# Optimization experiments

Measured on AMD Instinct MI355X. Metric: run time of the kernel, lower is better.

The kernel has to match this reference:

```python
import jax, jax.numpy as jnp
import numpy as np

_SAMPLING_EPS = 1e-5


def setup_inputs() -> dict:
    key = jax.random.key(0)
    k1, k2, k3, k4, k5 = jax.random.split(key, 5)
    B, V = 128, 128000
    logits = jax.random.normal(k1, (B, V), dtype=jnp.float32)
    temperature = jax.random.uniform(k2, (B,), dtype=jnp.float32)  # some rows < eps -> greedy
    top_k = jax.random.randint(k3, (B,), 1, 64, dtype=jnp.int32)   # in [1, 63]
    top_p = jax.random.uniform(k4, (B,), dtype=jnp.float32, minval=0.05, maxval=1.0)
    noise_u = jax.random.uniform(k5, (B, V), dtype=jnp.float32, minval=1e-10, maxval=1.0)
    return {"logits": logits, "temperature": temperature, "top_k": top_k,
            "top_p": top_p, "noise_u": noise_u, "max_num_logprobs": 5}


def _apply_top_k_top_p(logits, k, p):
    # Faithful to vLLM: ascending sort, top-k threshold mask, top-p cumsum mask, scatter back.
    B, V = logits.shape
    order = jnp.argsort(logits, axis=-1)                       # ascending, [B, V]
    logits_sort = jnp.take_along_axis(logits, order, axis=-1)
    neg_inf = jnp.float32(-jnp.inf)
    # top-k: pivot value at position V - k; everything strictly below it -> -inf
    pivot_idx = (V - k.astype(jnp.int32))[:, None]             # [B, 1]
    pivot = jnp.take_along_axis(logits_sort, pivot_idx, axis=-1)
    logits_sort = jnp.where(logits_sort < pivot, neg_inf, logits_sort)
    # top-p: softmax over sorted logits, cumsum, drop prefix with mass <= 1 - p (keep last)
    probs_sort = jax.nn.softmax(logits_sort, axis=-1)
    probs_sum = jnp.cumsum(probs_sort, axis=-1)
    top_p_mask = probs_sum <= (1.0 - p)[:, None]
    top_p_mask = top_p_mask.at[:, -1].set(False)
    logits_sort = jnp.where(top_p_mask, neg_inf, logits_sort)
    # scatter back to original vocab order
    rows = jnp.arange(B)[:, None]
    return jnp.zeros_like(logits).at[rows, order].set(logits_sort)


def reference(logits, temperature, top_k, top_p, noise_u, max_num_logprobs):
    # temperature scaling (temp < eps means greedy; divide by 1.0 instead)
    temp = jnp.where(temperature < _SAMPLING_EPS, 1.0, temperature)
    logits = logits.astype(jnp.float32) / temp[:, None]
    # top-k / top-p filtering
    logits = _apply_top_k_top_p(logits, top_k, top_p)
    # probabilities and sampling
    probs = jax.nn.softmax(logits, axis=-1)
    greedy = jnp.argmax(probs, axis=-1)
    q = -jnp.log(noise_u)                                      # Exp(1) noise (q.exponential_())
    random = jnp.argmax(probs / q, axis=-1)
    sampled = jnp.where(temperature < _SAMPLING_EPS, greedy, random).astype(jnp.int32)
    # top-k logprobs
    logprobs = jax.nn.log_softmax(logits, axis=-1)
    topk_logprobs, topk_indices = jax.lax.top_k(logprobs, max_num_logprobs)
    return sampled, topk_indices.astype(jnp.int32), topk_logprobs
```

## Files before the change

### kernel.cpp

```cpp
#include <hip/hip_runtime.h>
#include <math.h>
#include <stdint.h>

#define BT     256
#define NCHUNK 8
#define CAP    4096
#define TOPC   64
#define TILE   (BT * 8)
#define NC     (NCHUNK * TOPC)

__device__ __forceinline__ unsigned f2ord(float f) {
    unsigned u = __float_as_uint(f);
    return u ^ ((u & 0x80000000u) ? 0xFFFFFFFFu : 0x80000000u);
}
__device__ __forceinline__ float ord2f(unsigned k) {
    unsigned u = (k & 0x80000000u) ? (k ^ 0x80000000u) : (k ^ 0xFFFFFFFFu);
    return __uint_as_float(u);
}

__device__ unsigned radix_select_compact(unsigned* s_key, int* s_idx,
                                         unsigned* s_ckey, int* s_cidx,
                                         unsigned* s_hist, unsigned* p_cnt2,
                                         unsigned n, int tid)
{
    unsigned prefix = 0u;
    int remaining = TOPC;
    for (int shift = 28; shift >= 0; shift -= 4) {
        if (tid < 16) s_hist[tid] = 0u;
        __syncthreads();
        for (unsigned i = (unsigned)tid; i < n; i += BT) {
            unsigned k = s_key[i];
            bool ing = (shift == 28) || ((k >> (shift + 4)) == (prefix >> (shift + 4)));
            if (ing) atomicAdd(&s_hist[(k >> shift) & 15u], 1u);
        }
        __syncthreads();
        int cum = 0; int b = 0;
        for (int bb = 15; bb >= 0; --bb) {
            cum += (int)s_hist[bb];
            if (cum >= remaining) { b = bb; break; }
        }
        remaining -= (cum - (int)s_hist[b]);
        prefix |= ((unsigned)b) << shift;
        __syncthreads();
    }
    if (tid == 0) *p_cnt2 = 0u;
    __syncthreads();
    for (unsigned i = (unsigned)tid; i < n; i += BT) {
        unsigned k = s_key[i];
        if (k > prefix) {
            unsigned pos = atomicAdd(p_cnt2, 1u);
            s_ckey[pos] = k; s_cidx[pos] = s_idx[i];
        }
    }
    __syncthreads();
    for (unsigned i = (unsigned)tid; i < n; i += BT) {
        unsigned k = s_key[i];
        if (k == prefix) {
            unsigned pos = atomicAdd(p_cnt2, 1u);
            if (pos < TOPC) { s_ckey[pos] = k; s_cidx[pos] = s_idx[i]; }
        }
    }
    __syncthreads();
    return prefix;
}

__global__ __launch_bounds__(BT) void phase1_topk_chunks(
    const float* __restrict__ logits, uint2* __restrict__ cand,
    int V, int chunk_len)
{
    __shared__ unsigned s_key[CAP];
    __shared__ int      s_idx[CAP];
    __shared__ unsigned s_ckey[TOPC];
    __shared__ int      s_cidx[TOPC];
    __shared__ unsigned s_hist[16];
    __shared__ unsigned s_cnt, s_cnt2, s_thr;

    const int row   = blockIdx.y;
    const int chunk = blockIdx.x;
    const int tid   = threadIdx.x;
    const int lane  = tid & 63;
    const int c0    = chunk * chunk_len;
    int c1 = c0 + chunk_len; if (c1 > V) c1 = V;
    const float* rowp = logits + (size_t)row * (size_t)V;

    if (tid == 0) { s_cnt = 0u; s_thr = 0u; }
    __syncthreads();

    for (int t0 = c0; t0 < c1; t0 += TILE) {
        unsigned cnt = s_cnt;
        if (cnt + TILE > CAP) {
            unsigned vstar = radix_select_compact(s_key, s_idx, s_ckey, s_cidx,
                                                  s_hist, &s_cnt2, cnt, tid);
            if (tid < TOPC) { s_key[tid] = s_ckey[tid]; s_idx[tid] = s_cidx[tid]; }
            if (tid == 0)   { s_cnt = TOPC; s_thr = vstar; }
            __syncthreads();
        }
        unsigned thr = s_thr;
        int base = t0 + tid * 8;
        unsigned k[8];
        if (base < c1) {
            float4 a = *(const float4*)(rowp + base);
            float4 b = *(const float4*)(rowp + base + 4);
            k[0] = f2ord(a.x); k[1] = f2ord(a.y); k[2] = f2ord(a.z); k[3] = f2ord(a.w);
            k[4] = f2ord(b.x); k[5] = f2ord(b.y); k[6] = f2ord(b.z); k[7] = f2ord(b.w);
        } else {
            #pragma unroll
            for (int j = 0; j < 8; ++j) k[j] = 0u;
        }
        #pragma unroll
        for (int j = 0; j < 8; ++j) {
            bool pass = (k[j] > thr);
            unsigned long long mask = __ballot(pass);
            if (mask) {
                int leader = __ffsll((unsigned long long)mask) - 1;
                unsigned b0 = 0u;
                if (lane == leader)
                    b0 = atomicAdd(&s_cnt, (unsigned)__popcll(mask));
                b0 = __shfl(b0, leader);
                if (pass) {
                    unsigned pos = b0 + (unsigned)__popcll(mask & ((1ull << lane) - 1ull));
                    s_key[pos] = k[j];
                    s_idx[pos] = base + j;
                }
            }
        }
        __syncthreads();
    }

    unsigned cnt = s_cnt;
    radix_select_compact(s_key, s_idx, s_ckey, s_cidx, s_hist, &s_cnt2, cnt, tid);
    if (tid < TOPC) {
        cand[((size_t)row * NCHUNK + chunk) * TOPC + tid] =
            make_uint2(s_ckey[tid], (unsigned)s_cidx[tid]);
    }
}

__global__ __launch_bounds__(BT) void phase2_sample(
    const uint2* __restrict__ cand,
    const float* __restrict__ temperature,
    const int*   __restrict__ top_k,
    const float* __restrict__ top_p,
    const float* __restrict__ noise_u,
    float* __restrict__ out,
    int B, int V, int M)
{
    __shared__ unsigned key[NC];
    __shared__ int      idx[NC];
    __shared__ float    sval[TOPC], se[TOPC], sq[TOPC];
    __shared__ int      sidx[TOPC];

    const int r   = blockIdx.x;
    const int tid = threadIdx.x;

    for (int i = tid; i < NC; i += BT) {
        uint2 c = cand[(size_t)r * NC + i];
        key[i] = c.x; idx[i] = (int)c.y;
    }
    __syncthreads();

    for (int kk = 2; kk <= NC; kk <<= 1) {
        for (int j = kk >> 1; j > 0; j >>= 1) {
            int t  = tid;
            int i0 = ((t & ~(j - 1)) << 1) | (t & (j - 1));
            int i1 = i0 | j;
            bool up = ((i0 & kk) == 0);
            unsigned ka = key[i0], kb = key[i1];
            int ia = idx[i0], ib = idx[i1];
            bool gt = (ka > kb) || (ka == kb && ia < ib);
            if (gt == up) { key[i0] = kb; key[i1] = ka; idx[i0] = ib; idx[i1] = ia; }
            __syncthreads();
        }
    }

    float temp_orig = temperature[r];
    float temp = (temp_orig < 1e-5f) ? 1.0f : temp_orig;

    if (tid < TOPC) {
        unsigned k = key[NC - 1 - tid];
        int id = idx[NC - 1 - tid];
        sval[tid] = ord2f(k) / temp;
        sidx[tid] = id;
        float u = noise_u[(size_t)r * (size_t)V + id];
        sq[tid] = -logf(u);
    }
    __syncthreads();
    if (tid < TOPC) se[tid] = expf(sval[tid] - sval[0]);
    __syncthreads();

    if (tid == 0) {
        int k = top_k[r];
        if (k < 1) k = 1; if (k > TOPC) k = TOPC;
        float p = top_p[r];

        float pivot = sval[k - 1];
        int m = k;
        while (m < TOPC && sval[m] >= pivot) ++m;

        float sum = 0.f;
        for (int i = 0; i < m; ++i) sum += se[i];

        float thr1 = 1.0f - p;
        float S = 0.f;
        int f = 1;
        for (int i = m - 1; i >= 1; --i) {
            S += se[i] / sum;
            if (S > thr1) { f = i + 1; break; }
        }

        float sum2 = 0.f;
        for (int i = 0; i < f; ++i) sum2 += se[i];

        int greedy = sidx[0];
        float best = -1.f; int bidx = 0x7fffffff;
        for (int i = 0; i < f; ++i) {
            float ratio = (se[i] / sum2) / sq[i];
            if (ratio > best || (ratio == best && sidx[i] < bidx)) {
                best = ratio; bidx = sidx[i];
            }
        }
        int sampled = (temp_orig < 1e-5f) ? greedy : bidx;

        float lse = logf(sum2);
        out[r] = (float)sampled;
        float* oidx = out + B + (size_t)r * M;
        float* olp  = out + B + (size_t)B * M + (size_t)r * M;
        int produced = 0;
        for (int i = 0; i < f && produced < M; ++i, ++produced) {
            oidx[produced] = (float)sidx[i];
            olp[produced]  = (sval[i] - sval[0]) - lse;
        }
        int v = 0;
        while (produced < M) {
            bool used = false;
            for (int i = 0; i < f; ++i) if (sidx[i] == v) { used = true; break; }
            if (!used) { oidx[produced] = (float)v; olp[produced] = -3.0e38f; ++produced; }
            ++v;
        }
    }
}

extern "C" void kernel_launch(void* const* d_in, const int* in_sizes, int n_in,
                              void* d_out, int out_size, void* d_ws, size_t ws_size,
                              hipStream_t stream)
{
    const float* logits      = (const float*)d_in[0];
    const float* temperature = (const float*)d_in[1];
    const int*   top_k       = (const int*)d_in[2];
    const float* top_p       = (const float*)d_in[3];
    const float* noise_u     = (const float*)d_in[4];

    const int B = in_sizes[1];
    const int V = in_sizes[0] / B;
    const int M = (out_size / B - 1) / 2;

    uint2* cand = (uint2*)d_ws;

    int chunk_len = (((V + NCHUNK - 1) / NCHUNK) + 7) & ~7;

    dim3 g1(NCHUNK, B);
    phase1_topk_chunks<<<g1, BT, 0, stream>>>(logits, cand, V, chunk_len);
    phase2_sample<<<B, BT, 0, stream>>>(cand, temperature, top_k, top_p, noise_u,
                                        (float*)d_out, B, V, M);
}
```

Before: 187.4 us.

## Restructure chunk top-k: seed threshold from first tile, prefetch, packed buffers

Measured after the change: 181.9 us. 2.9% less time.

```diff
diff --git a/kernel.cpp b/kernel.cpp
--- a/kernel.cpp
+++ b/kernel.cpp
@@ -4,7 +4,7 @@
 
 #define BT     256
 #define NCHUNK 8
-#define CAP    4096
+#define CAP    2048
 #define TOPC   64
 #define TILE   (BT * 8)
 #define NC     (NCHUNK * TOPC)
@@ -18,46 +18,46 @@
     return __uint_as_float(u);
 }
 
-__device__ unsigned radix_select_compact(unsigned* s_key, int* s_idx,
-                                         unsigned* s_ckey, int* s_cidx,
-                                         unsigned* s_hist, unsigned* p_cnt2,
-                                         unsigned n, int tid)
+__device__ unsigned radix_select_compact(uint2* s_buf, uint2* s_keep,
+                                         unsigned (*s_hist)[16], unsigned* p_cnt2,
+                                         unsigned n, int tid, int wid)
 {
     unsigned prefix = 0u;
     int remaining = TOPC;
     for (int shift = 28; shift >= 0; shift -= 4) {
-        if (tid < 16) s_hist[tid] = 0u;
+        if (tid < 64) ((unsigned*)s_hist)[tid] = 0u;
         __syncthreads();
         for (unsigned i = (unsigned)tid; i < n; i += BT) {
-            unsigned k = s_key[i];
+            unsigned k = s_buf[i].x;
             bool ing = (shift == 28) || ((k >> (shift + 4)) == (prefix >> (shift + 4)));
-            if (ing) atomicAdd(&s_hist[(k >> shift) & 15u], 1u);
+            if (ing) atomicAdd(&s_hist[wid][(k >> shift) & 15u], 1u);
         }
         __syncthreads();
-        int cum = 0; int b = 0;
+        int cum = 0; int b = 0; unsigned hb = 0u;
         for (int bb = 15; bb >= 0; --bb) {
-            cum += (int)s_hist[bb];
-            if (cum >= remaining) { b = bb; break; }
-        }
-        remaining -= (cum - (int)s_hist[b]);
+            unsigned h = s_hist[0][bb] + s_hist[1][bb] + s_hist[2][bb] + s_hist[3][bb];
+            cum += (int)h;
+            if (cum >= remaining) { b = bb; hb = h; break; }
+        }
+        remaining -= (cum - (int)hb);
         prefix |= ((unsigned)b) << shift;
         __syncthreads();
     }
     if (tid == 0) *p_cnt2 = 0u;
     __syncthreads();
     for (unsigned i = (unsigned)tid; i < n; i += BT) {
-        unsigned k = s_key[i];
-        if (k > prefix) {
+        uint2 c = s_buf[i];
+        if (c.x > prefix) {
             unsigned pos = atomicAdd(p_cnt2, 1u);
-            s_ckey[pos] = k; s_cidx[pos] = s_idx[i];
+            s_keep[pos] = c;
         }
     }
     __syncthreads();
     for (unsigned i = (unsigned)tid; i < n; i += BT) {
-        unsigned k = s_key[i];
-        if (k == prefix) {
+        uint2 c = s_buf[i];
+        if (c.x == prefix) {
             unsigned pos = atomicAdd(p_cnt2, 1u);
-            if (pos < TOPC) { s_ckey[pos] = k; s_cidx[pos] = s_idx[i]; }
+            if (pos < TOPC) s_keep[pos] = c;
         }
     }
     __syncthreads();
@@ -68,35 +68,23 @@
     const float* __restrict__ logits, uint2* __restrict__ cand,
     int V, int chunk_len)
 {
-    __shared__ unsigned s_key[CAP];
-    __shared__ int      s_idx[CAP];
-    __shared__ unsigned s_ckey[TOPC];
-    __shared__ int      s_cidx[TOPC];
-    __shared__ unsigned s_hist[16];
-    __shared__ unsigned s_cnt, s_cnt2, s_thr;
+    __shared__ uint2    s_buf[CAP];
+    __shared__ uint2    s_keep[TOPC];
+    __shared__ unsigned s_hist[4][16];
+    __shared__ unsigned s_cnt, s_cnt2, s_thr, s_ovf;
 
     const int row   = blockIdx.y;
     const int chunk = blockIdx.x;
     const int tid   = threadIdx.x;
-    const int lane  = tid & 63;
+    const int wid   = tid >> 6;
     const int c0    = chunk * chunk_len;
     int c1 = c0 + chunk_len; if (c1 > V) c1 = V;
     const float* rowp = logits + (size_t)row * (size_t)V;
 
-    if (tid == 0) { s_cnt = 0u; s_thr = 0u; }
-    __syncthreads();
-
-    for (int t0 = c0; t0 < c1; t0 += TILE) {
-        unsigned cnt = s_cnt;
-        if (cnt + TILE > CAP) {
-            unsigned vstar = radix_select_compact(s_key, s_idx, s_ckey, s_cidx,
-                                                  s_hist, &s_cnt2, cnt, tid);
-            if (tid < TOPC) { s_key[tid] = s_ckey[tid]; s_idx[tid] = s_cidx[tid]; }
-            if (tid == 0)   { s_cnt = TOPC; s_thr = vstar; }
-            __syncthreads();
-        }
-        unsigned thr = s_thr;
-        int base = t0 + tid * 8;
+    if (tid == 0) s_ovf = 0u;
+
+    {
+        int base = c0 + tid * 8;
         unsigned k[8];
         if (base < c1) {
             float4 a = *(const float4*)(rowp + base);
@@ -109,30 +97,93 @@
         }
         #pragma unroll
         for (int j = 0; j < 8; ++j) {
-            bool pass = (k[j] > thr);
-            unsigned long long mask = __ballot(pass);
-            if (mask) {
-                int leader = __ffsll((unsigned long long)mask) - 1;
-                unsigned b0 = 0u;
-                if (lane == leader)
-                    b0 = atomicAdd(&s_cnt, (unsigned)__popcll(mask));
-                b0 = __shfl(b0, leader);
-                if (pass) {
-                    unsigned pos = b0 + (unsigned)__popcll(mask & ((1ull << lane) - 1ull));
-                    s_key[pos] = k[j];
-                    s_idx[pos] = base + j;
+            int id = (base < c1) ? (base + j) : c0;
+            s_buf[tid + j * BT] = make_uint2(k[j], (unsigned)id);
+        }
+    }
+    __syncthreads();
+    {
+        unsigned vst = radix_select_compact(s_buf, s_keep, s_hist, &s_cnt2,
+                                            CAP, tid, wid);
+        if (tid < TOPC) s_buf[tid] = s_keep[tid];
+        if (tid == 0) { s_cnt = TOPC; s_thr = vst; }
+        __syncthreads();
+    }
+
+    float4 a0 = {}, b0 = {}; bool v0 = false;
+    int t0 = c0 + TILE;
+    if (t0 < c1) {
+        int bs = t0 + tid * 8;
+        if (bs < c1) {
+            a0 = *(const float4*)(rowp + bs);
+            b0 = *(const float4*)(rowp + bs + 4);
+            v0 = true;
+        }
+    }
+    for (int t = t0; t < c1; t += TILE) {
+        float4 a1 = {}, b1 = {}; bool v1 = false;
+        int tn = t + TILE;
+        if (tn < c1) {
+            int bs = tn + tid * 8;
+            if (bs < c1) {
+                a1 = *(const float4*)(rowp + bs);
+                b1 = *(const float4*)(rowp + bs + 4);
+                v1 = true;
+            }
+        }
+        unsigned k[8];
+        if (v0) {
+            k[0] = f2ord(a0.x); k[1] = f2ord(a0.y); k[2] = f2ord(a0.z); k[3] = f2ord(a0.w);
+            k[4] = f2ord(b0.x); k[5] = f2ord(b0.y); k[6] = f2ord(b0.z); k[7] = f2ord(b0.w);
+        } else {
+            #pragma unroll
+            for (int j = 0; j < 8; ++j) k[j] = 0u;
+        }
+        const int base = t + tid * 8;
+        const unsigned thr = s_thr;
+        unsigned pm = 0u; int np = 0;
+        #pragma unroll
+        for (int j = 0; j < 8; ++j)
+            if (k[j] > thr) { pm |= (1u << j); ++np; }
+
+        for (;;) {
+            if (np) {
+                unsigned pos = atomicAdd(&s_cnt, (unsigned)np);
+                unsigned rem = 0u; int nr = 0;
+                #pragma unroll
+                for (int j = 0; j < 8; ++j) {
+                    if (pm & (1u << j)) {
+                        if (pos < CAP) s_buf[pos] = make_uint2(k[j], (unsigned)(base + j));
+                        else { rem |= (1u << j); ++nr; }
+                        ++pos;
+                    }
                 }
+                if (nr) s_ovf = 1u;
+                pm = rem; np = nr;
             }
-        }
-        __syncthreads();
-    }
-
-    unsigned cnt = s_cnt;
-    radix_select_compact(s_key, s_idx, s_ckey, s_cidx, s_hist, &s_cnt2, cnt, tid);
-    if (tid < TOPC) {
-        cand[((size_t)row * NCHUNK + chunk) * TOPC + tid] =
-            make_uint2(s_ckey[tid], (unsigned)s_cidx[tid]);
-    }
+            __syncthreads();
+            unsigned ovf = s_ovf;
+            __syncthreads();
+            if (!ovf) break;
+            unsigned n = s_cnt; if (n > CAP) n = CAP;
+            unsigned v2 = radix_select_compact(s_buf, s_keep, s_hist, &s_cnt2,
+                                               n, tid, wid);
+            if (tid < TOPC) s_buf[tid] = s_keep[tid];
+            if (tid == 0) { s_cnt = TOPC; s_thr = v2; s_ovf = 0u; }
+            __syncthreads();
+            unsigned rem = 0u; int nr = 0;
+            #pragma unroll
+            for (int j = 0; j < 8; ++j)
+                if ((pm & (1u << j)) && k[j] > v2) { rem |= (1u << j); ++nr; }
+            pm = rem; np = nr;
+        }
+        a0 = a1; b0 = b1; v0 = v1;
+    }
+
+    unsigned n = s_cnt;
+    radix_select_compact(s_buf, s_keep, s_hist, &s_cnt2, n, tid, wid);
+    if (tid < TOPC)
+        cand[((size_t)row * NCHUNK + chunk) * TOPC + tid] = s_keep[tid];
 }
 
 __global__ __launch_bounds__(BT) void phase2_sample(
```
